# Kernel tuning notes

Hardware: AMD Instinct MI355X
Metric: run time of the kernel (lower is better)

The kernel has to match this reference:

```python
import jax, jax.numpy as jnp
import numpy as np
from jax import lax

R, K = 1000, 80                 # proposals per image, foreground classes
IMG_H, IMG_W = 800.0, 1333.0    # image_shape (h, w) used by Boxes.clip
SCORE_THRESH = 0.05
NMS_THRESH = 0.5
TOPK = 100                      # topk_per_image


def setup_inputs() -> dict:
    key = jax.random.key(0)
    k1, k2, k3 = jax.random.split(key, 3)
    # well-formed class-specific boxes: x1y1 + positive wh
    x1y1 = jax.random.uniform(k1, (R, K, 2)) * jnp.array([IMG_W - 60.0, IMG_H - 60.0])
    wh = jax.random.uniform(k2, (R, K, 2)) * 200.0 + 10.0
    boxes = jnp.concatenate([x1y1, x1y1 + wh], axis=-1).reshape(R, K * 4)
    logits = jax.random.normal(k3, (R, K + 1)) * 2.0
    scores = jax.nn.softmax(logits, axis=-1)  # (R, K+1), last col = background
    return {"boxes": boxes, "scores": scores}


def _iou_matrix(b):
    # b: [R, 4] (x1, y1, x2, y2) -> [R, R] pairwise IoU
    x1, y1, x2, y2 = b[:, 0], b[:, 1], b[:, 2], b[:, 3]
    area = jnp.clip(x2 - x1, 0.0) * jnp.clip(y2 - y1, 0.0)
    xx1 = jnp.maximum(x1[:, None], x1[None, :])
    yy1 = jnp.maximum(y1[:, None], y1[None, :])
    xx2 = jnp.minimum(x2[:, None], x2[None, :])
    yy2 = jnp.minimum(y2[:, None], y2[None, :])
    inter = jnp.clip(xx2 - xx1, 0.0) * jnp.clip(yy2 - yy1, 0.0)
    union = area[:, None] + area[None, :] - inter
    return inter / jnp.maximum(union, 1e-9)


def _nms_one_class(boxes_c, scores_c, valid_c):
    # boxes_c: [R,4], scores_c: [R], valid_c: [R] bool (passed score filter)
    masked = jnp.where(valid_c, scores_c, -jnp.inf)
    order = jnp.argsort(-masked)            # descending score
    b = boxes_c[order]
    s = masked[order]
    v = valid_c[order]
    iou = iou_full = _iou_matrix(b)          # [R, R]
    idx = jnp.arange(R)

    def body(i, keep):
        # box i (if still kept & valid) suppresses later boxes with high IoU
        sup = (iou_full[i] > NMS_THRESH) & keep[i] & (idx > i)
        return keep & ~sup

    keep = lax.fori_loop(0, R, body, v)
    return s, keep, order


def reference(boxes, scores):
    # boxes: (R, K*4), scores: (R, K+1)
    bx = boxes.reshape(R, K, 4)
    # Boxes.clip(image_shape=(h, w)): x in [0, w], y in [0, h]
    bx = jnp.stack([
        jnp.clip(bx[..., 0], 0.0, IMG_W),
        jnp.clip(bx[..., 1], 0.0, IMG_H),
        jnp.clip(bx[..., 2], 0.0, IMG_W),
        jnp.clip(bx[..., 3], 0.0, IMG_H),
    ], axis=-1)

    fg = scores[:, :-1]                                  # (R, K) foreground scores
    thres = jnp.minimum(SCORE_THRESH, (fg.mean() + fg.max()) / 2.0)
    valid = fg > thres                                   # filter_mask

    # per-class batched NMS (equivalent to torchvision batched_nms)
    boxes_k = jnp.transpose(bx, (1, 0, 2))               # [K, R, 4]
    s_sorted, keep, order = jax.vmap(_nms_one_class)(boxes_k, fg.T, valid.T)

    flat = jnp.where(keep, s_sorted, -jnp.inf).reshape(-1)   # [K*R]
    topv, topi = lax.top_k(flat, TOPK)                   # keep[:topk], score-sorted
    cls = topi // R
    pos = topi % R
    prop = order[cls, pos]                               # original proposal index (filter_inds[:,0])
    ok = jnp.isfinite(topv)
    okf = ok.astype(boxes.dtype)

    box_out = bx[prop, cls] * okf[:, None]               # pred_boxes  [TOPK, 4]
    sc_out = jnp.where(ok, topv, 0.0)                    # scores      [TOPK]
    full_out = scores[prop] * okf[:, None]               # full_scores [TOPK, K+1]
    cls_out = (cls * ok).astype(boxes.dtype)             # pred_classes as float col

    # packed result: [boxes(4) | score(1) | class(1) | full_scores(K+1)]
    return jnp.concatenate([box_out, sc_out[:, None], cls_out[:, None], full_out], axis=1)
```

## Files before the change

kernel.cpp:

```cpp
#include <hip/hip_runtime.h>
#include <stdint.h>

typedef unsigned long long u64;
typedef unsigned int u32;

#define R_N 1000
#define K_N 80
#define NCOL 81
#define TOPK_N 100
#define OUT_W 87
#define IMG_W_ 1333.0f
#define IMG_H_ 800.0f
#define CSTR 100
#define CSTRP 101
#define NQUAD ((R_N * NCOL) / 4)
#define NMAX 448
#define WMAX 7
#define KM (K_N * CSTR)
#define POISON 0xAAAAAAAAu

__device__ __forceinline__ u32 f32_order(float f) {
    u32 u = __float_as_uint(f);
    return u ^ (((u32)((int)u >> 31)) | 0x80000000u);
}
__device__ __forceinline__ float f32_unorder(u32 o) {
    u32 u = (o & 0x80000000u) ? (o ^ 0x80000000u) : ~o;
    return __uint_as_float(u);
}

__device__ __forceinline__ void grid_barrier(u32* bar, u32 nblk) {
    __syncthreads();
    if (threadIdx.x == 0) {
        __threadfence();
        if (__hip_atomic_load(bar, __ATOMIC_RELAXED, __HIP_MEMORY_SCOPE_AGENT) == POISON)
            atomicCAS(bar, POISON, 0u);
        __hip_atomic_fetch_add(bar, 1u, __ATOMIC_ACQ_REL, __HIP_MEMORY_SCOPE_AGENT);
        while (__hip_atomic_load(bar, __ATOMIC_ACQUIRE, __HIP_MEMORY_SCOPE_AGENT) < nblk)
            __builtin_amdgcn_s_sleep(2);
    }
    __syncthreads();
}

struct P2 {
    float4 bx4[R_N];
    u64 key_s[R_N];
    u64 pool[NMAX * WMAX];
    float area[R_N];
    float sc[R_N];
    u64 keep_words[16];
    int s_n;
};
struct P3 {
    u64 keys[K_N * CSTRP];
    int rnk[TOPK_N];
};
union SMEM { P2 p2; P3 p3; };

__global__ __launch_bounds__(256, 1) void k_all(const float* __restrict__ boxes,
                                                const float* __restrict__ scores,
                                                float* __restrict__ hdr,
                                                u32* __restrict__ bars,
                                                u64* __restrict__ cand,
                                                float* __restrict__ outp) {
    __shared__ SMEM sm;
    __shared__ float s_sum[4], s_max[4];
    __shared__ int s_cnt[4];
    __shared__ float s_thres;

    const int bid = blockIdx.x, tid = threadIdx.x;
    const int lane = tid & 63, wv = tid >> 6;
    const int c = bid;
    const u64 below = (lane == 0) ? 0ull : (~0ull >> (64 - lane));

    for (int r = tid; r < R_N; r += 256) sm.p2.sc[r] = scores[r * NCOL + c];

    {
        float sum = 0.f, mx = -1e30f;
        int q = bid * 256 + tid;
        if (q < NQUAD) {
            float4 v = ((const float4*)scores)[q];
            int m = (q * 4) % NCOL;
            float vv[4] = {v.x, v.y, v.z, v.w};
#pragma unroll
            for (int e = 0; e < 4; ++e) {
                int mm = m + e; if (mm >= NCOL) mm -= NCOL;
                if (mm != K_N) { sum += vv[e]; mx = fmaxf(mx, vv[e]); }
            }
        }
#pragma unroll
        for (int off = 32; off > 0; off >>= 1) {
            sum += __shfl_down(sum, off);
            mx = fmaxf(mx, __shfl_down(mx, off));
        }
        if (lane == 0) { s_sum[wv] = sum; s_max[wv] = mx; }
        __syncthreads();
        if (tid == 0) {
            hdr[2 * bid] = s_sum[0] + s_sum[1] + s_sum[2] + s_sum[3];
            hdr[2 * bid + 1] = fmaxf(fmaxf(s_max[0], s_max[1]), fmaxf(s_max[2], s_max[3]));
        }
    }

    float th = 0.05f;
    for (int pass = 0; ; ++pass) {
        u64* ukey = sm.p2.pool;
        if (wv == 0) {
            int nn = 0;
            for (int r0 = 0; r0 < R_N; r0 += 64) {
                int r = r0 + lane;
                bool pred = (r < R_N) && (sm.p2.sc[r] > th);
                u64 m = __ballot(pred);
                if (pred) {
                    int slot = nn + __popcll(m & below);
                    ukey[slot] = ((u64)f32_order(sm.p2.sc[r]) << 32) | (u64)(u32)(R_N - 1 - r);
                }
                nn += __popcll(m);
            }
            if (lane == 0) sm.p2.s_n = nn;
        }
        __syncthreads();
        const int n = sm.p2.s_n;

        for (int j = tid; j < n; j += 256) {
            u64 kj = ukey[j];
            int rank = 0;
            for (int k = 0; k < n; ++k) rank += (ukey[k] > kj) ? 1 : 0;
            int r = (R_N - 1) - (int)(kj & 0xFFFFFFFFull);
            float4 b = ((const float4*)boxes)[r * K_N + c];
            float x1 = fminf(fmaxf(b.x, 0.f), IMG_W_);
            float y1 = fminf(fmaxf(b.y, 0.f), IMG_H_);
            float x2 = fminf(fmaxf(b.z, 0.f), IMG_W_);
            float y2 = fminf(fmaxf(b.w, 0.f), IMG_H_);
            sm.p2.key_s[rank] = kj;
            sm.p2.bx4[rank] = make_float4(x1, y1, x2, y2);
            sm.p2.area[rank] = fmaxf(x2 - x1, 0.f) * fmaxf(y2 - y1, 0.f);
        }
        __syncthreads();

        if (n <= NMAX) {
            const int W = (n + 63) >> 6;
            u64* Mrow = sm.p2.pool;
            const int nh = n >> 1;
            for (int t2 = wv; t2 < 2 * W; t2 += 4) {
                int w = t2 >> 1, ih = t2 & 1;
                int i0 = ih ? nh : 0;
                int i1 = ih ? n : nh;
                int j = w * 64 + lane;
                bool jv = j < n;
                float4 bj = jv ? sm.p2.bx4[j] : make_float4(0.f, 0.f, 0.f, 0.f);
                float aj = jv ? sm.p2.area[j] : 0.f;
                for (int i = i0; i < i1; ++i) {
                    float4 bi = sm.p2.bx4[i];
                    float ai = sm.p2.area[i];
                    float xx1 = fmaxf(bi.x, bj.x), yy1 = fmaxf(bi.y, bj.y);
                    float xx2 = fminf(bi.z, bj.z), yy2 = fminf(bi.w, bj.w);
                    float inter = fmaxf(xx2 - xx1, 0.f) * fmaxf(yy2 - yy1, 0.f);
                    bool sup = jv && (j > i) &&
                               (inter / fmaxf(ai + aj - inter, 1e-9f) > 0.5f);
                    u64 m = __ballot(sup);
                    if (lane == 0) Mrow[i * W + w] = m;
                }
            }
            __syncthreads();

            if (wv == 0) {
                u64 keep_w = 0;
                if (lane < W) {
                    int rem = n - lane * 64;
                    keep_w = (rem >= 64) ? ~0ull : ((1ull << rem) - 1ull);
                }
                const int lw = (lane < W) ? lane : 0;
                u64 fifo[8];
#pragma unroll
                for (int d = 0; d < 8; ++d) fifo[d] = (d < n) ? Mrow[d * W + lw] : 0ull;
                for (int ib = 0; ib < n; ib += 8) {
#pragma unroll
                    for (int d = 0; d < 8; ++d) {
                        int i = ib + d;
                        if (i >= n) break;
                        u64 row = fifo[d];
                        int ip = i + 8;
                        fifo[d] = (ip < n) ? Mrow[ip * W + lw] : 0ull;
                        u64 kw = __shfl(keep_w, i >> 6);
                        if ((kw >> (i & 63)) & 1ull) keep_w &= ~row;
                    }
                }
                if (lane < W) sm.p2.keep_words[lane] = keep_w;
                if (lane >= W && lane < 16) sm.p2.keep_words[lane] = 0;
            }
        } else {
            int* keep = (int*)sm.p2.pool;
            for (int j = tid; j < n; j += 256) keep[j] = 1;
            __syncthreads();
            for (int i = 0; i < n - 1; ++i) {
                __syncthreads();
                if (!keep[i]) continue;
                float4 bi = sm.p2.bx4[i];
                float ai = sm.p2.area[i];
                for (int j = i + 1 + tid; j < n; j += 256) {
                    if (!keep[j]) continue;
                    float xx1 = fmaxf(bi.x, sm.p2.bx4[j].x), yy1 = fmaxf(bi.y, sm.p2.bx4[j].y);
                    float xx2 = fminf(bi.z, sm.p2.bx4[j].z), yy2 = fminf(bi.w, sm.p2.bx4[j].w);
                    float inter = fmaxf(xx2 - xx1, 0.f) * fmaxf(yy2 - yy1, 0.f);
                    if (inter / fmaxf(ai + sm.p2.area[j] - inter, 1e-9f) > 0.5f) keep[j] = 0;
                }
            }
            __syncthreads();
            if (wv == 0) {
                for (int w = 0; w < 16; ++w) {
                    int j = w * 64 + lane;
                    u64 m = __ballot((j < n) && keep[j]);
                    if (lane == 0) sm.p2.keep_words[w] = m;
                }
            }
        }
        __syncthreads();

        if (wv == 0) {
            int kb = 0;
            for (int j0 = 0; j0 < n; j0 += 64) {
                int j = j0 + lane;
                u64 mw = sm.p2.keep_words[j0 >> 6];
                bool kp = (j < n) && ((mw >> lane) & 1ull);
                u64 mm = __ballot(kp);
                int kr = kb + __popcll(mm & below);
                if (kp && kr < CSTR) {
                    u64 kj = sm.p2.key_s[j];
                    u32 osc = (u32)(kj >> 32);
                    int rr = (R_N - 1) - (int)(kj & 0xFFFFFFFFull);
                    int flat = c * R_N + j;
                    cand[c * CSTR + kr] =
                        ((u64)osc << 27) | ((u64)(u32)(131071 - flat) << 10) | (u64)(u32)rr;
                }
                kb += __popcll(mm);
            }
            if (kb > CSTR) kb = CSTR;
            for (int k2 = kb + lane; k2 < CSTR; k2 += 64) cand[c * CSTR + k2] = 0;
        }

        if (pass == 0) {
            grid_barrier(&bars[0], K_N);
            if (wv == 0) {
                float S = hdr[2 * lane], M = hdr[2 * lane + 1];
                if (lane + 64 < K_N) {
                    S += hdr[2 * (lane + 64)];
                    M = fmaxf(M, hdr[2 * (lane + 64) + 1]);
                }
#pragma unroll
                for (int off = 32; off > 0; off >>= 1) {
                    S += __shfl_down(S, off);
                    M = fmaxf(M, __shfl_down(M, off));
                }
                if (lane == 0)
                    s_thres = fminf(0.05f, 0.5f * (S / (float)(R_N * K_N) + M));
            }
            __syncthreads();
            if (s_thres == 0.05f) break;
            th = s_thres;
        } else {
            grid_barrier(&bars[1], K_N);
            break;
        }
    }

    {
        const ulonglong2* cp = (const ulonglong2*)cand;
        int cnt = 0;
        for (int t = tid; t < KM / 2; t += 256) {
            ulonglong2 v = cp[t];
            int e0 = 2 * t;
            int cc = e0 / CSTR, pos = e0 - cc * CSTR;
            sm.p3.keys[cc * CSTRP + pos] = v.x;
            sm.p3.keys[cc * CSTRP + pos + 1] = v.y;
            cnt += (v.x != 0ull) + (v.y != 0ull);
        }
#pragma unroll
        for (int off = 32; off > 0; off >>= 1) cnt += __shfl_down(cnt, off);
        if (lane == 0) s_cnt[wv] = cnt;
        if (tid < TOPK_N) sm.p3.rnk[tid] = tid;
        __syncthreads();
        const int total = s_cnt[0] + s_cnt[1] + s_cnt[2] + s_cnt[3];
        const int target = total < TOPK_N ? total : TOPK_N;

        for (int g = 0; g < 4; ++g) {
            int lo[8], hi[8], ii[8], base[8];
            u64 xv[8];
            bool act[8];
#pragma unroll
            for (int s = 0; s < 8; ++s) {
                int t = tid + 256 * (g * 8 + s);
                act[s] = t < CSTR * (K_N - 1);
                int i = act[s] ? (t / (K_N - 1)) : 0;
                int cc = act[s] ? (t - i * (K_N - 1)) : 0;
                cc += (cc >= c);
                ii[s] = i;
                base[s] = cc * CSTRP;
                xv[s] = sm.p3.keys[c * CSTRP + i];
                if (xv[s] == 0ull) act[s] = false;
                lo[s] = 0; hi[s] = CSTR;
            }
#pragma unroll
            for (int st = 0; st < 7; ++st) {
#pragma unroll
                for (int s = 0; s < 8; ++s) {
                    int mid = (lo[s] + hi[s]) >> 1;
                    u64 v = sm.p3.keys[base[s] + mid];
                    bool live = lo[s] < hi[s];
                    bool gt = live && (v > xv[s]);
                    lo[s] = gt ? mid + 1 : lo[s];
                    hi[s] = (live && !gt) ? mid : hi[s];
                }
            }
#pragma unroll
            for (int s = 0; s < 8; ++s)
                if (act[s] && lo[s] > 0) atomicAdd(&sm.p3.rnk[ii[s]], lo[s]);
        }
        __syncthreads();

        if (tid < CSTR) {
            u64 x = sm.p3.keys[c * CSTRP + tid];
            int r = sm.p3.rnk[tid];
            if (x != 0ull && r < target) {
                int prop = (int)(x & 0x3FFull);
                float score = f32_unorder((u32)((x >> 27) & 0xFFFFFFFFull));
                int ob = r * OUT_W;
                float4 bx = ((const float4*)boxes)[prop * K_N + c];
                outp[ob + 0] = fminf(fmaxf(bx.x, 0.f), IMG_W_);
                outp[ob + 1] = fminf(fmaxf(bx.y, 0.f), IMG_H_);
                outp[ob + 2] = fminf(fmaxf(bx.z, 0.f), IMG_W_);
                outp[ob + 3] = fminf(fmaxf(bx.w, 0.f), IMG_H_);
                outp[ob + 4] = score;
                outp[ob + 5] = (float)c;
                const int sb = prop * NCOL;
#pragma unroll 9
                for (int j = 0; j < NCOL; ++j) outp[ob + 6 + j] = scores[sb + j];
            }
        }
        for (int row = target + bid; row < TOPK_N; row += K_N) {
            int ob = row * OUT_W;
            for (int e = tid; e < OUT_W; e += 256) outp[ob + e] = 0.f;
        }
    }
}

extern "C" void kernel_launch(void* const* d_in, const int* in_sizes, int n_in,
                              void* d_out, int out_size, void* d_ws, size_t ws_size,
                              hipStream_t stream) {
    const float* boxes = (const float*)d_in[0];
    const float* scores = (const float*)d_in[1];
    float* hdr = (float*)d_ws;
    u32* bars = (u32*)((char*)d_ws + 768);
    u64* cand = (u64*)((char*)d_ws + 1024);

    k_all<<<dim3(K_N), dim3(256), 0, stream>>>(boxes, scores, hdr, bars, cand, (float*)d_out);
}
```

Baseline: 105.9 us.

## Parallelize compaction, split IoU rows four ways, narrow merge keys, spread output writes

Compaction of above-threshold proposals now uses all four waves with a prefix over per-wave counts, where before a single wave did it serially. The IoU mask build splits row ranges into quarters instead of halves for more wave parallelism. The final cross-class rank merge binary-searches 32-bit high key halves over only the nonzero candidates, resolving ties from global memory. Output rows are written cooperatively by all threads with coalesced per-column stores. These changes add more barriers and extra tie-resolution loads from global memory.

After: 109.3 us. +3.2%, slower.

```diff
diff --git a/kernel.cpp b/kernel.cpp
--- a/kernel.cpp
+++ b/kernel.cpp
@@ -12,7 +12,7 @@
 #define IMG_W_ 1333.0f
 #define IMG_H_ 800.0f
 #define CSTR 100
-#define CSTRP 101
+#define SHI 101
 #define NQUAD ((R_N * NCOL) / 4)
 #define NMAX 448
 #define WMAX 7
@@ -48,11 +48,14 @@
     float area[R_N];
     float sc[R_N];
     u64 keep_words[16];
-    int s_n;
 };
 struct P3 {
-    u64 keys[K_N * CSTRP];
+    u32 khi[K_N * SHI];
+    u32 klo_own[CSTR];
     int rnk[TOPK_N];
+    u64 wx[TOPK_N];
+    int wr[TOPK_N];
+    int wn;
 };
 union SMEM { P2 p2; P3 p3; };
 
@@ -64,7 +67,7 @@
                                                 float* __restrict__ outp) {
     __shared__ SMEM sm;
     __shared__ float s_sum[4], s_max[4];
-    __shared__ int s_cnt[4];
+    __shared__ int s_cnt[4], s_wcnt[4], s_kb[2];
     __shared__ float s_thres;
 
     const int bid = blockIdx.x, tid = threadIdx.x;
@@ -103,22 +106,32 @@
     float th = 0.05f;
     for (int pass = 0; ; ++pass) {
         u64* ukey = sm.p2.pool;
-        if (wv == 0) {
-            int nn = 0;
-            for (int r0 = 0; r0 < R_N; r0 += 64) {
-                int r = r0 + lane;
+        {
+            u64 m[4]; int wcnt = 0;
+#pragma unroll
+            for (int k = 0; k < 4; ++k) {
+                int r = wv * 256 + k * 64 + lane;
                 bool pred = (r < R_N) && (sm.p2.sc[r] > th);
-                u64 m = __ballot(pred);
+                m[k] = __ballot(pred);
+                wcnt += __popcll(m[k]);
+            }
+            if (lane == 0) s_wcnt[wv] = wcnt;
+            __syncthreads();
+            int run = 0;
+            for (int w2 = 0; w2 < wv; ++w2) run += s_wcnt[w2];
+#pragma unroll
+            for (int k = 0; k < 4; ++k) {
+                int r = wv * 256 + k * 64 + lane;
+                bool pred = (r < R_N) && (sm.p2.sc[r] > th);
                 if (pred) {
-                    int slot = nn + __popcll(m & below);
+                    int slot = run + __popcll(m[k] & below);
                     ukey[slot] = ((u64)f32_order(sm.p2.sc[r]) << 32) | (u64)(u32)(R_N - 1 - r);
                 }
-                nn += __popcll(m);
-            }
-            if (lane == 0) sm.p2.s_n = nn;
-        }
-        __syncthreads();
-        const int n = sm.p2.s_n;
+                run += __popcll(m[k]);
+            }
+        }
+        __syncthreads();
+        const int n = s_wcnt[0] + s_wcnt[1] + s_wcnt[2] + s_wcnt[3];
 
         for (int j = tid; j < n; j += 256) {
             u64 kj = ukey[j];
@@ -139,11 +152,11 @@
         if (n <= NMAX) {
             const int W = (n + 63) >> 6;
             u64* Mrow = sm.p2.pool;
-            const int nh = n >> 1;
-            for (int t2 = wv; t2 < 2 * W; t2 += 4) {
-                int w = t2 >> 1, ih = t2 & 1;
-                int i0 = ih ? nh : 0;
-                int i1 = ih ? n : nh;
+            const int q1 = n >> 2, q2 = n >> 1, q3 = (3 * n) >> 2;
+            for (int t2 = wv; t2 < 4 * W; t2 += 4) {
+                int w = t2 >> 2, qh = t2 & 3;
+                int i0 = (qh == 0) ? 0 : (qh == 1) ? q1 : (qh == 2) ? q2 : q3;
+                int i1 = (qh == 0) ? q1 : (qh == 1) ? q2 : (qh == 2) ? q3 : n;
                 int j = w * 64 + lane;
                 bool jv = j < n;
                 float4 bj = jv ? sm.p2.bx4[j] : make_float4(0.f, 0.f, 0.f, 0.f);
@@ -269,71 +282,112 @@
             ulonglong2 v = cp[t];
             int e0 = 2 * t;
             int cc = e0 / CSTR, pos = e0 - cc * CSTR;
-            sm.p3.keys[cc * CSTRP + pos] = v.x;
-            sm.p3.keys[cc * CSTRP + pos + 1] = v.y;
+            sm.p3.khi[cc * SHI + pos] = (u32)(v.x >> 32);
+            sm.p3.khi[cc * SHI + pos + 1] = (u32)(v.y >> 32);
+            if (cc == c) {
+                sm.p3.klo_own[pos] = (u32)v.x;
+                sm.p3.klo_own[pos + 1] = (u32)v.y;
+            }
             cnt += (v.x != 0ull) + (v.y != 0ull);
         }
+        if (tid < K_N) sm.p3.khi[tid * SHI + CSTR] = 0;
 #pragma unroll
         for (int off = 32; off > 0; off >>= 1) cnt += __shfl_down(cnt, off);
         if (lane == 0) s_cnt[wv] = cnt;
         if (tid < TOPK_N) sm.p3.rnk[tid] = tid;
+        if (tid == 0) sm.p3.wn = 0;
         __syncthreads();
         const int total = s_cnt[0] + s_cnt[1] + s_cnt[2] + s_cnt[3];
         const int target = total < TOPK_N ? total : TOPK_N;
 
-        for (int g = 0; g < 4; ++g) {
-            int lo[8], hi[8], ii[8], base[8];
-            u64 xv[8];
+        if (wv < 2) {
+            int t = wv * 64 + lane;
+            bool nz = (t < CSTR) && (sm.p3.khi[c * SHI + t] != 0);
+            u64 m = __ballot(nz);
+            if (lane == 0) s_kb[wv] = __popcll(m);
+        }
+        __syncthreads();
+        const int kb = s_kb[0] + s_kb[1];
+
+        const int TASKS = kb * (K_N - 1);
+        const int NG = (TASKS + 2047) / 2048;
+        for (int g = 0; g < NG; ++g) {
+            int lo1[8], hi1[8], lo2[8], hi2[8], base[8], cbase[8], ii[8];
+            u32 xhi[8], xlo[8];
             bool act[8];
 #pragma unroll
             for (int s = 0; s < 8; ++s) {
-                int t = tid + 256 * (g * 8 + s);
-                act[s] = t < CSTR * (K_N - 1);
+                int t = g * 2048 + s * 256 + tid;
+                act[s] = t < TASKS;
                 int i = act[s] ? (t / (K_N - 1)) : 0;
                 int cc = act[s] ? (t - i * (K_N - 1)) : 0;
                 cc += (cc >= c);
                 ii[s] = i;
-                base[s] = cc * CSTRP;
-                xv[s] = sm.p3.keys[c * CSTRP + i];
-                if (xv[s] == 0ull) act[s] = false;
-                lo[s] = 0; hi[s] = CSTR;
+                base[s] = cc * SHI;
+                cbase[s] = cc * CSTR;
+                xhi[s] = sm.p3.khi[c * SHI + i];
+                xlo[s] = sm.p3.klo_own[i];
+                lo1[s] = 0; hi1[s] = CSTR;
+                lo2[s] = 0; hi2[s] = CSTR;
             }
 #pragma unroll
             for (int st = 0; st < 7; ++st) {
 #pragma unroll
                 for (int s = 0; s < 8; ++s) {
-                    int mid = (lo[s] + hi[s]) >> 1;
-                    u64 v = sm.p3.keys[base[s] + mid];
-                    bool live = lo[s] < hi[s];
-                    bool gt = live && (v > xv[s]);
-                    lo[s] = gt ? mid + 1 : lo[s];
-                    hi[s] = (live && !gt) ? mid : hi[s];
-                }
-            }
-#pragma unroll
-            for (int s = 0; s < 8; ++s)
-                if (act[s] && lo[s] > 0) atomicAdd(&sm.p3.rnk[ii[s]], lo[s]);
-        }
-        __syncthreads();
-
-        if (tid < CSTR) {
-            u64 x = sm.p3.keys[c * CSTRP + tid];
+                    int m1 = (lo1[s] + hi1[s]) >> 1;
+                    u32 v1 = sm.p3.khi[base[s] + m1];
+                    bool l1 = lo1[s] < hi1[s];
+                    bool g1 = l1 && (v1 > xhi[s]);
+                    lo1[s] = g1 ? m1 + 1 : lo1[s];
+                    hi1[s] = (l1 && !g1) ? m1 : hi1[s];
+                    int m2 = (lo2[s] + hi2[s]) >> 1;
+                    u32 v2 = sm.p3.khi[base[s] + m2];
+                    bool l2 = lo2[s] < hi2[s];
+                    bool g2 = l2 && (v2 >= xhi[s]);
+                    lo2[s] = g2 ? m2 + 1 : lo2[s];
+                    hi2[s] = (l2 && !g2) ? m2 : hi2[s];
+                }
+            }
+#pragma unroll
+            for (int s = 0; s < 8; ++s) {
+                if (!act[s]) continue;
+                int add = lo1[s];
+                for (int j = lo1[s]; j < lo2[s]; ++j)
+                    add += ((u32)cand[cbase[s] + j] > xlo[s]) ? 1 : 0;
+                if (add > 0) atomicAdd(&sm.p3.rnk[ii[s]], add);
+            }
+        }
+        __syncthreads();
+
+        if (tid < kb) {
             int r = sm.p3.rnk[tid];
-            if (x != 0ull && r < target) {
-                int prop = (int)(x & 0x3FFull);
-                float score = f32_unorder((u32)((x >> 27) & 0xFFFFFFFFull));
-                int ob = r * OUT_W;
-                float4 bx = ((const float4*)boxes)[prop * K_N + c];
-                outp[ob + 0] = fminf(fmaxf(bx.x, 0.f), IMG_W_);
-                outp[ob + 1] = fminf(fmaxf(bx.y, 0.f), IMG_H_);
-                outp[ob + 2] = fminf(fmaxf(bx.z, 0.f), IMG_W_);
-                outp[ob + 3] = fminf(fmaxf(bx.w, 0.f), IMG_H_);
-                outp[ob + 4] = score;
-                outp[ob + 5] = (float)c;
-                const int sb = prop * NCOL;
-#pragma unroll 9
-                for (int j = 0; j < NCOL; ++j) outp[ob + 6 + j] = scores[sb + j];
-            }
+            if (r < target) {
+                int idx = atomicAdd(&sm.p3.wn, 1);
+                sm.p3.wx[idx] = ((u64)sm.p3.khi[c * SHI + tid] << 32) | (u64)sm.p3.klo_own[tid];
+                sm.p3.wr[idx] = r;
+            }
+        }
+        __syncthreads();
+        const int wn = sm.p3.wn;
+
+        for (int e = tid; e < wn * OUT_W; e += 256) {
+            int w = e / OUT_W, col = e - w * OUT_W;
+            u64 x = sm.p3.wx[w];
+            int r = sm.p3.wr[w];
+            int prop = (int)(x & 0x3FFull);
+            float val;
+            if (col < 4) {
+                float b = boxes[prop * (K_N * 4) + c * 4 + col];
+                float lim = (col & 1) ? IMG_H_ : IMG_W_;
+                val = fminf(fmaxf(b, 0.f), lim);
+            } else if (col == 4) {
+                val = f32_unorder((u32)((x >> 27) & 0xFFFFFFFFull));
+            } else if (col == 5) {
+                val = (float)c;
+            } else {
+                val = scores[prop * NCOL + (col - 6)];
+            }
+            outp[r * OUT_W + col] = val;
         }
         for (int row = target + bid; row < TOPK_N; row += K_N) {
             int ob = row * OUT_W;
```
